# Optimization experiments

Measured on AMD Instinct MI355X. Metric: run time of the kernel, lower is better.

## Reference

```python
import jax, jax.numpy as jnp
import numpy as np


def setup_inputs() -> dict:
    key = jax.random.key(0)
    k1, k2, k3 = jax.random.split(key, 3)
    B, C, D, S = 16, 80, 1024, 14  # batch, num_classes, feature dim, conv size
    return {
        "batch_size": B,
        "img_feature_map": jax.random.normal(k1, (B, D, S, S), dtype=jnp.float32),
        "word_features": jax.random.normal(k2, (C, D), dtype=jnp.float32),
        "fc_a_w": jax.random.normal(k3, (D,), dtype=jnp.float32) / np.float32(np.sqrt(D)),
        "fc_a_b": jnp.zeros((), dtype=jnp.float32),
    }


def reference(batch_size, img_feature_map, word_features, fc_a_w, fc_a_b):
    # img_feature_map: [B, D, H, W] -> [B, H, W, D]
    img = jnp.transpose(img_feature_map, (0, 2, 3, 1))
    # class-wise gated feature: tanh(img * word) -> [B, H, W, C, D]
    gated = jnp.tanh(img[:, :, :, None, :] * word_features[None, None, None, :, :])
    # rank-1 linear score: [B, H, W, C]
    scores = jnp.einsum('bhwcd,d->bhwc', gated, fc_a_w) + fc_a_b
    B, H, W, C = scores.shape
    # softmax over spatial positions (H*W) per (batch, class)
    coef = jax.nn.softmax(scores.reshape(B, H * W, C), axis=1).reshape(B, H, W, C)
    # attention-weighted spatial pooling -> [B, C, D]
    return jnp.einsum('bhwc,bhwd->bcd', coef, img)
```

## Files before the change

kernel.cpp:

```cpp
#include <hip/hip_runtime.h>

#define BB 16
#define CC 80
#define DD 1024
#define HW 196
#define NSP (BB * HW)
#define NCH 8
#define DCH 128
#define CPB 4
#define NCQ (CC / CPB)
#define TWO_LOG2E 2.8853900817779268f

__global__ __launch_bounds__(256) void scores_k(const float* __restrict__ img,
                                                const float* __restrict__ word,
                                                const float* __restrict__ fa,
                                                float* __restrict__ partial,
                                                float* __restrict__ imgT) {
    const int g = blockIdx.x * 256 + threadIdx.x;
    if (g >= NSP) return;
    const int b  = g / HW;
    const int hw = g - b * HW;
    const int d0 = blockIdx.y * DCH;
    const int c0 = blockIdx.z * CPB;

    const float* ip = img + ((size_t)b * DD + d0) * HW + hw;

    float p[CPB];
#pragma unroll
    for (int k = 0; k < CPB; ++k) p[k] = 0.f;

    for (int q = 0; q < DCH / 32; ++q) {
        float iv[32];
        const float* qp = ip + (size_t)q * 32 * HW;
#pragma unroll
        for (int i = 0; i < 32; ++i)
            iv[i] = qp[(size_t)i * HW];

        if (blockIdx.z == 0) {
            float4* tp = (float4*)(imgT + (size_t)g * DD + d0 + q * 32);
#pragma unroll
            for (int i = 0; i < 8; ++i)
                tp[i] = make_float4(iv[4 * i], iv[4 * i + 1], iv[4 * i + 2], iv[4 * i + 3]);
        }

#pragma unroll
        for (int i = 0; i < 32; ++i)
            iv[i] *= TWO_LOG2E;

        const float* fp = fa + d0 + q * 32;
#pragma unroll
        for (int k = 0; k < CPB; ++k) {
            const float* wp = word + (size_t)(c0 + k) * DD + d0 + q * 32;
            float p0 = 0.f, p1 = 0.f;
#pragma unroll
            for (int i = 0; i < 32; i += 2) {
                float y0 = iv[i]     * wp[i];
                float y1 = iv[i + 1] * wp[i + 1];
                float e0 = __builtin_amdgcn_exp2f(y0);
                float e1 = __builtin_amdgcn_exp2f(y1);
                float r0 = __builtin_amdgcn_rcpf(e0 + 1.f);
                float r1 = __builtin_amdgcn_rcpf(e1 + 1.f);
                p0 = fmaf(fp[i],     r0, p0);
                p1 = fmaf(fp[i + 1], r1, p1);
            }
            p[k] += p0 + p1;
        }
    }

#pragma unroll
    for (int k = 0; k < CPB; ++k)
        partial[(((size_t)b * NCH + blockIdx.y) * CC + (c0 + k)) * HW + hw]
            = (-TWO_LOG2E) * p[k];
}

__global__ __launch_bounds__(256) void pool2_k(const float* __restrict__ imgT,
                                               const float* __restrict__ partial,
                                               float* __restrict__ out) {
    __shared__ float ct[4 * HW];
    const int b   = blockIdx.x;
    const int dt0 = blockIdx.y * 256;
    const int cg  = blockIdx.z * 4;
    const int t   = threadIdx.x;
    const int w   = t >> 6, l = t & 63;

    {
        const int c = cg + w;
        float x0 = 0.f, x1 = 0.f, x2 = 0.f, x3 = 0.f;
#pragma unroll
        for (int ch = 0; ch < NCH; ++ch) {
            const float* pp = partial + (((size_t)b * NCH + ch) * CC + c) * HW;
            x0 += pp[l];
            x1 += pp[l + 64];
            x2 += pp[l + 128];
            if (l < HW - 192) x3 += pp[l + 192];
        }
        float x3m = (l < HW - 192) ? x3 : -3.4e38f;

        float m = fmaxf(fmaxf(x0, x1), fmaxf(x2, x3m));
#pragma unroll
        for (int off = 32; off >= 1; off >>= 1) m = fmaxf(m, __shfl_xor(m, off, 64));

        float e0 = __builtin_amdgcn_exp2f(x0 - m);
        float e1 = __builtin_amdgcn_exp2f(x1 - m);
        float e2 = __builtin_amdgcn_exp2f(x2 - m);
        float e3 = (l < HW - 192) ? __builtin_amdgcn_exp2f(x3 - m) : 0.f;

        float s = (e0 + e1) + (e2 + e3);
#pragma unroll
        for (int off = 32; off >= 1; off >>= 1) s += __shfl_xor(s, off, 64);

        float inv = __builtin_amdgcn_rcpf(s);
        float* cr = ct + w * HW;
        cr[l]       = e0 * inv;
        cr[l + 64]  = e1 * inv;
        cr[l + 128] = e2 * inv;
        if (l < HW - 192) cr[l + 192] = e3 * inv;
    }
    __syncthreads();

    const float* ib = imgT + (size_t)b * HW * DD + dt0 + t;

    float a0 = 0.f, a1 = 0.f, a2 = 0.f, a3 = 0.f;
#pragma unroll 7
    for (int h = 0; h < HW; h += 4) {
        float i0 = ib[(size_t)(h    ) * DD];
        float i1 = ib[(size_t)(h + 1) * DD];
        float i2 = ib[(size_t)(h + 2) * DD];
        float i3 = ib[(size_t)(h + 3) * DD];
        float4 c0v = *(const float4*)(ct + h);
        float4 c1v = *(const float4*)(ct + HW + h);
        float4 c2v = *(const float4*)(ct + 2 * HW + h);
        float4 c3v = *(const float4*)(ct + 3 * HW + h);
        a0 = fmaf(c0v.x, i0, fmaf(c0v.y, i1, fmaf(c0v.z, i2, fmaf(c0v.w, i3, a0))));
        a1 = fmaf(c1v.x, i0, fmaf(c1v.y, i1, fmaf(c1v.z, i2, fmaf(c1v.w, i3, a1))));
        a2 = fmaf(c2v.x, i0, fmaf(c2v.y, i1, fmaf(c2v.z, i2, fmaf(c2v.w, i3, a2))));
        a3 = fmaf(c3v.x, i0, fmaf(c3v.y, i1, fmaf(c3v.z, i2, fmaf(c3v.w, i3, a3))));
    }

    float* ob = out + ((size_t)b * CC + cg) * DD + dt0 + t;
    ob[0]              = a0;
    ob[DD]             = a1;
    ob[2 * (size_t)DD] = a2;
    ob[3 * (size_t)DD] = a3;
}

extern "C" void kernel_launch(void* const* d_in, const int* in_sizes, int n_in,
                              void* d_out, int out_size, void* d_ws, size_t ws_size,
                              hipStream_t stream) {
    const float* img  = (const float*)d_in[1];
    const float* word = (const float*)d_in[2];
    const float* fa   = (const float*)d_in[3];
    float* out = (float*)d_out;

    float* partial = (float*)d_ws;
    float* imgT    = partial + (size_t)BB * NCH * CC * HW;

    scores_k<<<dim3((NSP + 255) / 256, NCH, NCQ), 256, 0, stream>>>(img, word, fa, partial, imgT);
    pool2_k<<<dim3(BB, DD / 256, CC / 4), 256, 0, stream>>>(imgT, partial, out);
}
```

Measured before the change: 148.9 us.

## Split softmax into its own kernel and pool 8 classes per block

The softmax over spatial positions moves into a separate kernel that runs once per (batch, class) and writes coefficients in place into the partial buffer. Before, it was recomputed in every d-tile block. The pooling kernel then reads coefficients from global memory and accumulates 8 classes per thread, which halves how often the transposed image is re-read. The cost is an extra kernel launch and loading coefficients from global/cache instead of LDS.

Result: slower. 168.4 us (+13.1%).

```diff
diff --git a/kernel.cpp b/kernel.cpp
--- a/kernel.cpp
+++ b/kernel.cpp
@@ -9,6 +9,7 @@
 #define DCH 128
 #define CPB 4
 #define NCQ (CC / CPB)
+#define PCPB 8
 #define TWO_LOG2E 2.8853900817779268f
 
 __global__ __launch_bounds__(256) void scores_k(const float* __restrict__ img,
@@ -73,75 +74,75 @@
             = (-TWO_LOG2E) * p[k];
 }
 
-__global__ __launch_bounds__(256) void pool2_k(const float* __restrict__ imgT,
-                                               const float* __restrict__ partial,
+__global__ __launch_bounds__(256) void softmax_k(float* partial) {
+    const int idx = blockIdx.x * 4 + (threadIdx.x >> 6);
+    const int l   = threadIdx.x & 63;
+    const int b   = idx / CC;
+    const int c   = idx - b * CC;
+
+    float x0 = 0.f, x1 = 0.f, x2 = 0.f, x3 = 0.f;
+#pragma unroll
+    for (int ch = 0; ch < NCH; ++ch) {
+        const float* pp = partial + (((size_t)b * NCH + ch) * CC + c) * HW;
+        x0 += pp[l];
+        x1 += pp[l + 64];
+        x2 += pp[l + 128];
+        if (l < HW - 192) x3 += pp[l + 192];
+    }
+    float x3m = (l < HW - 192) ? x3 : -3.4e38f;
+
+    float m = fmaxf(fmaxf(x0, x1), fmaxf(x2, x3m));
+#pragma unroll
+    for (int off = 32; off >= 1; off >>= 1) m = fmaxf(m, __shfl_xor(m, off, 64));
+
+    float e0 = __builtin_amdgcn_exp2f(x0 - m);
+    float e1 = __builtin_amdgcn_exp2f(x1 - m);
+    float e2 = __builtin_amdgcn_exp2f(x2 - m);
+    float e3 = (l < HW - 192) ? __builtin_amdgcn_exp2f(x3 - m) : 0.f;
+
+    float s = (e0 + e1) + (e2 + e3);
+#pragma unroll
+    for (int off = 32; off >= 1; off >>= 1) s += __shfl_xor(s, off, 64);
+
+    float inv = __builtin_amdgcn_rcpf(s);
+    float* cr = partial + (((size_t)b * NCH) * CC + c) * HW;
+    cr[l]       = e0 * inv;
+    cr[l + 64]  = e1 * inv;
+    cr[l + 128] = e2 * inv;
+    if (l < HW - 192) cr[l + 192] = e3 * inv;
+}
+
+__global__ __launch_bounds__(128) void pool3_k(const float* __restrict__ imgT,
+                                               const float* __restrict__ coef,
                                                float* __restrict__ out) {
-    __shared__ float ct[4 * HW];
-    const int b   = blockIdx.x;
-    const int dt0 = blockIdx.y * 256;
-    const int cg  = blockIdx.z * 4;
-    const int t   = threadIdx.x;
-    const int w   = t >> 6, l = t & 63;
+    const int b  = blockIdx.x;
+    const int d  = blockIdx.y * 128 + threadIdx.x;
+    const int c0 = blockIdx.z * PCPB;
 
-    {
-        const int c = cg + w;
-        float x0 = 0.f, x1 = 0.f, x2 = 0.f, x3 = 0.f;
+    const float* ib = imgT + (size_t)b * HW * DD + d;
+    const float* cb = coef + (((size_t)b * NCH) * CC + c0) * HW;
+
+    float acc[PCPB];
 #pragma unroll
-        for (int ch = 0; ch < NCH; ++ch) {
-            const float* pp = partial + (((size_t)b * NCH + ch) * CC + c) * HW;
-            x0 += pp[l];
-            x1 += pp[l + 64];
-            x2 += pp[l + 128];
-            if (l < HW - 192) x3 += pp[l + 192];
-        }
-        float x3m = (l < HW - 192) ? x3 : -3.4e38f;
+    for (int k = 0; k < PCPB; ++k) acc[k] = 0.f;
 
-        float m = fmaxf(fmaxf(x0, x1), fmaxf(x2, x3m));
-#pragma unroll
-        for (int off = 32; off >= 1; off >>= 1) m = fmaxf(m, __shfl_xor(m, off, 64));
-
-        float e0 = __builtin_amdgcn_exp2f(x0 - m);
-        float e1 = __builtin_amdgcn_exp2f(x1 - m);
-        float e2 = __builtin_amdgcn_exp2f(x2 - m);
-        float e3 = (l < HW - 192) ? __builtin_amdgcn_exp2f(x3 - m) : 0.f;
-
-        float s = (e0 + e1) + (e2 + e3);
-#pragma unroll
-        for (int off = 32; off >= 1; off >>= 1) s += __shfl_xor(s, off, 64);
-
-        float inv = __builtin_amdgcn_rcpf(s);
-        float* cr = ct + w * HW;
-        cr[l]       = e0 * inv;
-        cr[l + 64]  = e1 * inv;
-        cr[l + 128] = e2 * inv;
-        if (l < HW - 192) cr[l + 192] = e3 * inv;
-    }
-    __syncthreads();
-
-    const float* ib = imgT + (size_t)b * HW * DD + dt0 + t;
-
-    float a0 = 0.f, a1 = 0.f, a2 = 0.f, a3 = 0.f;
 #pragma unroll 7
     for (int h = 0; h < HW; h += 4) {
         float i0 = ib[(size_t)(h    ) * DD];
         float i1 = ib[(size_t)(h + 1) * DD];
         float i2 = ib[(size_t)(h + 2) * DD];
         float i3 = ib[(size_t)(h + 3) * DD];
-        float4 c0v = *(const float4*)(ct + h);
-        float4 c1v = *(const float4*)(ct + HW + h);
-        float4 c2v = *(const float4*)(ct + 2 * HW + h);
-        float4 c3v = *(const float4*)(ct + 3 * HW + h);
-        a0 = fmaf(c0v.x, i0, fmaf(c0v.y, i1, fmaf(c0v.z, i2, fmaf(c0v.w, i3, a0))));
-        a1 = fmaf(c1v.x, i0, fmaf(c1v.y, i1, fmaf(c1v.z, i2, fmaf(c1v.w, i3, a1))));
-        a2 = fmaf(c2v.x, i0, fmaf(c2v.y, i1, fmaf(c2v.z, i2, fmaf(c2v.w, i3, a2))));
-        a3 = fmaf(c3v.x, i0, fmaf(c3v.y, i1, fmaf(c3v.z, i2, fmaf(c3v.w, i3, a3))));
+#pragma unroll
+        for (int k = 0; k < PCPB; ++k) {
+            float4 cv = *(const float4*)(cb + (size_t)k * HW + h);
+            acc[k] = fmaf(cv.x, i0, fmaf(cv.y, i1, fmaf(cv.z, i2, fmaf(cv.w, i3, acc[k]))));
+        }
     }
 
-    float* ob = out + ((size_t)b * CC + cg) * DD + dt0 + t;
-    ob[0]              = a0;
-    ob[DD]             = a1;
-    ob[2 * (size_t)DD] = a2;
-    ob[3 * (size_t)DD] = a3;
+    float* ob = out + ((size_t)b * CC + c0) * DD + d;
+#pragma unroll
+    for (int k = 0; k < PCPB; ++k)
+        ob[(size_t)k * DD] = acc[k];
 }
 
 extern "C" void kernel_launch(void* const* d_in, const int* in_sizes, int n_in,
@@ -156,5 +157,6 @@
     float* imgT    = partial + (size_t)BB * NCH * CC * HW;
 
     scores_k<<<dim3((NSP + 255) / 256, NCH, NCQ), 256, 0, stream>>>(img, word, fa, partial, imgT);
-    pool2_k<<<dim3(BB, DD / 256, CC / 4), 256, 0, stream>>>(imgT, partial, out);
+    softmax_k<<<dim3(BB * CC / 4), 256, 0, stream>>>(partial);
+    pool3_k<<<dim3(BB, DD / 128, CC / PCPB), 128, 0, stream>>>(imgT, partial, out);
 }
```
